# Optimization experiments

Measured on AMD Instinct MI355X. Metric: run time of the kernel, lower is better.

## Reference

```python
import jax, jax.numpy as jnp
import numpy as np

WINDOW = 128
BACKWARD = 1
FORWARD = 0

def look_around(x, pad_value):
    # x: [b, windows, window_size, ...]; pad window axis and gather shifted windows
    w = x.shape[1]
    pads = [(0, 0), (BACKWARD, FORWARD)] + [(0, 0)] * (x.ndim - 2)
    p = jnp.pad(x, pads, constant_values=pad_value)
    return jnp.concatenate([p[:, i:i + w] for i in range(BACKWARD + FORWARD + 1)], axis=2)

def setup_inputs() -> dict:
    key = jax.random.key(0)
    ks = jax.random.split(key, 5)
    shp = (2, 16, 4096, 64)
    names = ['q', 'k', 'q_rot', 'k_rot', 'v']
    inp = {n: jax.random.normal(ks[i], shp, dtype=jnp.float32) for i, n in enumerate(names)}
    inp['states'] = 0
    inp['inferring_states'] = 0
    return inp

def reference(q, k, q_rot, k_rot, v, states, inferring_states):
    shape = q.shape
    merge = lambda t: t.reshape(-1, t.shape[-2], t.shape[-1])
    q, k, q_rot, k_rot, v = map(merge, (q, k, q_rot, k_rot, v))
    b, t, e = q.shape
    windows = t // WINDOW
    ticker = jnp.arange(t, dtype=q.dtype)[None, :]
    b_t = ticker.reshape(1, windows, WINDOW)
    bucket = lambda x: x.reshape(b, windows, WINDOW, e)
    bq, bk, bq_rot, bk_rot, bv = map(bucket, (q, k, q_rot, k_rot, v))
    bk = look_around(bk, 0.0)
    bk_rot = look_around(bk_rot, 0.0)
    bv = look_around(bv, 0.0)
    bq_t = b_t
    bq_k = look_around(b_t, -1.0)
    scale = e ** (-0.5)
    dots = jnp.einsum('bwie,bwje->bwij', bq, bk) * scale
    dots_rot = jnp.einsum('bwie,bwje->bwij', bq_rot, bk_rot) * scale
    mask_value = -jnp.finfo(dots.dtype).max
    causal_mask = bq_t[:, :, :, None] < bq_k[:, :, None, :]
    pad_mask = bq_k[:, :, None, :] == -1
    mask = causal_mask | pad_mask
    dots = jnp.where(mask, mask_value, dots)
    dots_rot = jnp.where(mask, mask_value, dots_rot)
    attn = jax.nn.softmax(dots + dots_rot, axis=-1)
    out = jnp.einsum('bwij,bwje->bwie', attn, bv)
    return out.reshape(shape)
```

## Files before the change

### kernel.cpp

```cpp
#include <hip/hip_runtime.h>
#include <stdint.h>

#define T 4096
#define E 64
#define NBH 32
#define NWIN 32
#define LDKS 128
#define LDVS 64
#define KK_ELEMS (64*LDKS)
#define VT_ELEMS (64*LDVS)
#define BUF_ELEMS (KK_ELEMS+VT_ELEMS)
#define SMEM_BYTES (2*BUF_ELEMS*2)

typedef __attribute__((ext_vector_type(8))) short short8;
typedef __attribute__((ext_vector_type(4))) short short4v;
typedef __attribute__((ext_vector_type(4))) float f32x4;

__device__ __forceinline__ short f2bf(float x) {
  unsigned u = __float_as_uint(x);
  u += 0x7fffu + ((u >> 16) & 1u);
  return (short)(u >> 16);
}

__device__ __forceinline__ unsigned cvtpk(float lo, float hi) {
  unsigned r;
  asm("v_cvt_pk_bf16_f32 %0, %1, %2" : "=v"(r) : "v"(lo), "v"(hi));
  return r;
}

__device__ __forceinline__ void block_sync_lds() {
  asm volatile("s_waitcnt lgkmcnt(0)" ::: "memory");
  __builtin_amdgcn_s_barrier();
  asm volatile("" ::: "memory");
}

struct SubStage { float4 sk[4]; float sv[8]; };

__device__ __forceinline__ void sub_issue(SubStage& st,
    const float* __restrict__ k, const float* __restrict__ kr,
    const float* __restrict__ v, size_t rowbase, int tid, int wid, int lane) {
#pragma unroll
  for (int m = 0; m < 2; ++m) {
    const float* src = m ? kr : k;
#pragma unroll
    for (int it = 0; it < 2; ++it) {
      int idx = it * 512 + tid;
      st.sk[m * 2 + it] = *(const float4*)(src + (rowbase + (idx >> 4)) * E + (idx & 15) * 4);
    }
  }
  const float* vp = v + (rowbase + wid * 8) * E + lane;
#pragma unroll
  for (int i = 0; i < 8; ++i) st.sv[i] = vp[(size_t)i * E];
}

__device__ __forceinline__ void sub_commit(const SubStage& st,
    short* __restrict__ KK, short* __restrict__ Vt, int tid, int wid, int lane) {
#pragma unroll
  for (int m = 0; m < 2; ++m)
#pragma unroll
    for (int it = 0; it < 2; ++it) {
      int idx = it * 512 + tid;
      int row = idx >> 4;
      int chunk = m * 8 + ((idx & 15) >> 1);
      float4 f = st.sk[m * 2 + it];
      short4v h = { f2bf(f.x), f2bf(f.y), f2bf(f.z), f2bf(f.w) };
      *(short4v*)(KK + row * LDKS + ((chunk ^ (row & 15)) << 3) + (idx & 1) * 4) = h;
    }
#pragma unroll
  for (int rq = 0; rq < 2; ++rq) {
    short4v h = { f2bf(st.sv[rq*4+0]), f2bf(st.sv[rq*4+1]),
                  f2bf(st.sv[rq*4+2]), f2bf(st.sv[rq*4+3]) };
    *(short4v*)(Vt + lane * LDVS + ((wid ^ (lane & 7)) << 3) + rq * 4) = h;
  }
}

__device__ __forceinline__ void q_issue(float4* sq,
    const float* __restrict__ q, const float* __restrict__ qr,
    size_t rbase, int w, int wid, int li, int lg) {
  const size_t qrow = rbase + (size_t)w * 128 + wid * 16 + li;
#pragma unroll
  for (int kt = 0; kt < 4; ++kt) {
    const float* sp = (kt < 2 ? q : qr) + qrow * E + (kt & 1) * 32 + lg * 8;
    sq[kt * 2 + 0] = *(const float4*)sp;
    sq[kt * 2 + 1] = *(const float4*)(sp + 4);
  }
}

__device__ __forceinline__ void q_commit(const float4* sq, short8* aF) {
#pragma unroll
  for (int kt = 0; kt < 4; ++kt) {
    float4 f0 = sq[kt * 2], f1 = sq[kt * 2 + 1];
    short8 a;
    a[0]=f2bf(f0.x*0.125f); a[1]=f2bf(f0.y*0.125f); a[2]=f2bf(f0.z*0.125f); a[3]=f2bf(f0.w*0.125f);
    a[4]=f2bf(f1.x*0.125f); a[5]=f2bf(f1.y*0.125f); a[6]=f2bf(f1.z*0.125f); a[7]=f2bf(f1.w*0.125f);
    aF[kt] = a;
  }
}

__global__ __launch_bounds__(512, 4)
void la_attn(const float* __restrict__ qg, const float* __restrict__ kg,
             const float* __restrict__ qrg, const float* __restrict__ krg,
             const float* __restrict__ vg, float* __restrict__ outg) {
  extern __shared__ short smem[];

  const int lid = blockIdx.y * NWIN + blockIdx.x;
  const int wl  = (lid & 7) * 128 + (lid >> 3);
  const int win = wl & (NWIN - 1), bh = wl >> 5;

  const int tid = threadIdx.x;
  const int wid = tid >> 6, lane = tid & 63;
  const int li = lane & 15, lg = lane >> 4;
  const size_t rbase = (size_t)bh * T;
  const int q_i = wid * 16 + li;

  short8 aF[4];
  SubStage st;

  const int s0 = (win == 0) ? 2 : 0;
#define KROW(s) (rbase + (size_t)(win * 128 + ((s) - 2) * 64))

  {
    SubStage stA;
    float4 sq[8];
    sub_issue(stA, kg, krg, vg, KROW(s0), tid, wid, lane);
    q_issue(sq, qg, qrg, rbase, win, wid, li, lg);
    sub_commit(stA, smem, smem + KK_ELEMS, tid, wid, lane);
    q_commit(sq, aF);
    if (s0 + 1 < 4) sub_issue(st, kg, krg, vg, KROW(s0 + 1), tid, wid, lane);
  }
  block_sync_lds();

  float m = -1e30f, l = 0.f;
  f32x4 O[4] = {{0,0,0,0},{0,0,0,0},{0,0,0,0},{0,0,0,0}};

  for (int s = s0; s < 4; ++s) {
    const int cur = (s - s0) & 1;
    short* KKc = smem + cur * BUF_ELEMS;
    short* Vtc = KKc + KK_ELEMS;

    if (s + 1 < 4) {
      sub_commit(st, smem + (cur ^ 1) * BUF_ELEMS,
                 smem + (cur ^ 1) * BUF_ELEMS + KK_ELEMS, tid, wid, lane);
      if (s + 2 < 4) sub_issue(st, kg, krg, vg, KROW(s + 2), tid, wid, lane);
      asm volatile("" ::: "memory");
    }

    f32x4 p[4];
#pragma unroll
    for (int ct = 0; ct < 4; ++ct) {
      f32x4 acc = {0.f, 0.f, 0.f, 0.f};
      const int row = ct * 16 + li;
#pragma unroll
      for (int kt = 0; kt < 4; ++kt) {
        const short* kb = KKc + row * LDKS + (((kt * 4 + lg) ^ li) << 3);
        acc = __builtin_amdgcn_mfma_f32_16x16x32_bf16(*(const short8*)kb, aF[kt], acc, 0, 0, 0);
      }
      p[ct] = acc;
    }

    if (s >= 2) {
      const int joff = (s - 2) * 64 + lg * 4;
#pragma unroll
      for (int ct = 0; ct < 4; ++ct)
#pragma unroll
        for (int r = 0; r < 4; ++r)
          if (joff + ct * 16 + r > q_i) p[ct][r] = -1e30f;
    }
    float mx = -1e30f;
#pragma unroll
    for (int ct = 0; ct < 4; ++ct)
#pragma unroll
      for (int r = 0; r < 4; ++r) mx = fmaxf(mx, p[ct][r]);
    mx = fmaxf(mx, __shfl_xor(mx, 16));
    mx = fmaxf(mx, __shfl_xor(mx, 32));
    const float mn = fmaxf(m, mx);
    const float f = __expf(m - mn);
    float sm = 0.f;
#pragma unroll
    for (int ct = 0; ct < 4; ++ct)
#pragma unroll
      for (int r = 0; r < 4; ++r) {
        float e = __expf(p[ct][r] - mn);
        p[ct][r] = e;
        sm += e;
      }
    sm += __shfl_xor(sm, 16);
    sm += __shfl_xor(sm, 32);
    l = l * f + sm;
    m = mn;
#pragma unroll
    for (int nt = 0; nt < 4; ++nt)
#pragma unroll
      for (int r = 0; r < 4; ++r) O[nt][r] *= f;

    unsigned W0[4], W1[4];
#pragma unroll
    for (int ct = 0; ct < 4; ++ct) {
      W0[ct] = cvtpk(p[ct][0], p[ct][1]);
      W1[ct] = cvtpk(p[ct][2], p[ct][3]);
    }

    const bool lowhalf = (lg < 2);
    const bool sendR = (lg == 0) | (lg == 3);
#pragma unroll
    for (int kt = 0; kt < 2; ++kt) {
      const int cA = kt * 2, cB = cA + 1;
      unsigned P0 = lowhalf ? W0[cB] : W0[cA];
      unsigned P1 = lowhalf ? W1[cB] : W1[cA];
      unsigned R0 = __shfl_xor(P0, 32);
      unsigned R1 = __shfl_xor(P1, 32);
      unsigned L0 = lowhalf ? W0[cA] : W0[cB];
      unsigned L1 = lowhalf ? W1[cA] : W1[cB];
      unsigned S0 = sendR ? R0 : L0;
      unsigned S1 = sendR ? R1 : L1;
      unsigned T0 = __shfl_xor(S0, 16);
      unsigned T1 = __shfl_xor(S1, 16);
      unsigned F0 = (lg == 0) ? L0 : ((lg == 2) ? R0 : T0);
      unsigned F1 = (lg == 0) ? L1 : ((lg == 2) ? R1 : T1);
      unsigned G0 = (lg == 1) ? R0 : ((lg == 3) ? L0 : T0);
      unsigned G1 = (lg == 1) ? R1 : ((lg == 3) ? L1 : T1);
      union { unsigned u[4]; short8 s; } bu;
      bu.u[0] = F0; bu.u[1] = F1; bu.u[2] = G0; bu.u[3] = G1;
      const short8 bP = bu.s;
#pragma unroll
      for (int nt = 0; nt < 4; ++nt) {
        const short* vb = Vtc + (nt * 16 + li) * LDVS + (((kt * 4 + lg) ^ (li & 7)) << 3);
        O[nt] = __builtin_amdgcn_mfma_f32_16x16x32_bf16(*(const short8*)vb, bP, O[nt], 0, 0, 0);
      }
    }

    block_sync_lds();
  }

  const float linv = 1.f / l;
  float* op = outg + (rbase + (size_t)win * 128 + wid * 16 + li) * E + lg * 4;
#pragma unroll
  for (int nt = 0; nt < 4; ++nt) {
    float4 o = { O[nt][0] * linv, O[nt][1] * linv, O[nt][2] * linv, O[nt][3] * linv };
    *(float4*)(op + nt * 16) = o;
  }
#undef KROW
}

extern "C" void kernel_launch(void* const* d_in, const int* in_sizes, int n_in,
                              void* d_out, int out_size, void* d_ws, size_t ws_size,
                              hipStream_t stream) {
  const float* q  = (const float*)d_in[0];
  const float* k  = (const float*)d_in[1];
  const float* qr = (const float*)d_in[2];
  const float* kr = (const float*)d_in[3];
  const float* v  = (const float*)d_in[4];
  float* out = (float*)d_out;
  la_attn<<<dim3(NWIN, NBH), 512, SMEM_BYTES, stream>>>(q, k, qr, kr, v, out);
}
```

Baseline: 201.3 us.

## Drop LDS staging; read K directly, pre-transpose V to bf16 in separate kernel

```diff
diff --git a/kernel.cpp b/kernel.cpp
--- a/kernel.cpp
+++ b/kernel.cpp
@@ -5,15 +5,8 @@
 #define E 64
 #define NBH 32
 #define NWIN 32
-#define LDKS 128
-#define LDVS 64
-#define KK_ELEMS (64*LDKS)
-#define VT_ELEMS (64*LDVS)
-#define BUF_ELEMS (KK_ELEMS+VT_ELEMS)
-#define SMEM_BYTES (2*BUF_ELEMS*2)
 
 typedef __attribute__((ext_vector_type(8))) short short8;
-typedef __attribute__((ext_vector_type(4))) short short4v;
 typedef __attribute__((ext_vector_type(4))) float f32x4;
 
 __device__ __forceinline__ short f2bf(float x) {
@@ -28,218 +21,207 @@
   return r;
 }
 
-__device__ __forceinline__ void block_sync_lds() {
-  asm volatile("s_waitcnt lgkmcnt(0)" ::: "memory");
-  __builtin_amdgcn_s_barrier();
-  asm volatile("" ::: "memory");
-}
-
-struct SubStage { float4 sk[4]; float sv[8]; };
-
-__device__ __forceinline__ void sub_issue(SubStage& st,
-    const float* __restrict__ k, const float* __restrict__ kr,
-    const float* __restrict__ v, size_t rowbase, int tid, int wid, int lane) {
-#pragma unroll
-  for (int m = 0; m < 2; ++m) {
-    const float* src = m ? kr : k;
-#pragma unroll
-    for (int it = 0; it < 2; ++it) {
-      int idx = it * 512 + tid;
-      st.sk[m * 2 + it] = *(const float4*)(src + (rowbase + (idx >> 4)) * E + (idx & 15) * 4);
-    }
-  }
-  const float* vp = v + (rowbase + wid * 8) * E + lane;
-#pragma unroll
-  for (int i = 0; i < 8; ++i) st.sv[i] = vp[(size_t)i * E];
-}
-
-__device__ __forceinline__ void sub_commit(const SubStage& st,
-    short* __restrict__ KK, short* __restrict__ Vt, int tid, int wid, int lane) {
-#pragma unroll
-  for (int m = 0; m < 2; ++m)
-#pragma unroll
-    for (int it = 0; it < 2; ++it) {
-      int idx = it * 512 + tid;
-      int row = idx >> 4;
-      int chunk = m * 8 + ((idx & 15) >> 1);
-      float4 f = st.sk[m * 2 + it];
-      short4v h = { f2bf(f.x), f2bf(f.y), f2bf(f.z), f2bf(f.w) };
-      *(short4v*)(KK + row * LDKS + ((chunk ^ (row & 15)) << 3) + (idx & 1) * 4) = h;
-    }
-#pragma unroll
-  for (int rq = 0; rq < 2; ++rq) {
-    short4v h = { f2bf(st.sv[rq*4+0]), f2bf(st.sv[rq*4+1]),
-                  f2bf(st.sv[rq*4+2]), f2bf(st.sv[rq*4+3]) };
-    *(short4v*)(Vt + lane * LDVS + ((wid ^ (lane & 7)) << 3) + rq * 4) = h;
-  }
-}
-
-__device__ __forceinline__ void q_issue(float4* sq,
-    const float* __restrict__ q, const float* __restrict__ qr,
-    size_t rbase, int w, int wid, int li, int lg) {
-  const size_t qrow = rbase + (size_t)w * 128 + wid * 16 + li;
-#pragma unroll
-  for (int kt = 0; kt < 4; ++kt) {
-    const float* sp = (kt < 2 ? q : qr) + qrow * E + (kt & 1) * 32 + lg * 8;
-    sq[kt * 2 + 0] = *(const float4*)sp;
-    sq[kt * 2 + 1] = *(const float4*)(sp + 4);
-  }
-}
-
-__device__ __forceinline__ void q_commit(const float4* sq, short8* aF) {
-#pragma unroll
-  for (int kt = 0; kt < 4; ++kt) {
-    float4 f0 = sq[kt * 2], f1 = sq[kt * 2 + 1];
-    short8 a;
-    a[0]=f2bf(f0.x*0.125f); a[1]=f2bf(f0.y*0.125f); a[2]=f2bf(f0.z*0.125f); a[3]=f2bf(f0.w*0.125f);
-    a[4]=f2bf(f1.x*0.125f); a[5]=f2bf(f1.y*0.125f); a[6]=f2bf(f1.z*0.125f); a[7]=f2bf(f1.w*0.125f);
-    aF[kt] = a;
-  }
-}
-
-__global__ __launch_bounds__(512, 4)
+__device__ __forceinline__ short8 pack8(float4 f0, float4 f1) {
+  union { unsigned u[4]; short8 s8; } r;
+  r.u[0] = cvtpk(f0.x, f0.y); r.u[1] = cvtpk(f0.z, f0.w);
+  r.u[2] = cvtpk(f1.x, f1.y); r.u[3] = cvtpk(f1.z, f1.w);
+  return r.s8;
+}
+
+__device__ __forceinline__ short8 pack8s(float4 f0, float4 f1, float s) {
+  union { unsigned u[4]; short8 s8; } r;
+  r.u[0] = cvtpk(f0.x*s, f0.y*s); r.u[1] = cvtpk(f0.z*s, f0.w*s);
+  r.u[2] = cvtpk(f1.x*s, f1.y*s); r.u[3] = cvtpk(f1.z*s, f1.w*s);
+  return r.s8;
+}
+
+__global__ __launch_bounds__(256)
+void v_transpose(const float* __restrict__ vg, short* __restrict__ vt) {
+  __shared__ float tile[64][65];
+  const int bh = blockIdx.y;
+  const int t0 = blockIdx.x * 64;
+  const int tid = threadIdx.x;
+  const int c = tid & 63, r4 = tid >> 6;
+  const float* src = vg + ((size_t)bh * T + t0) * E;
+#pragma unroll
+  for (int i = 0; i < 16; ++i) {
+    int r = i * 4 + r4;
+    tile[r][c] = src[(size_t)r * E + c];
+  }
+  __syncthreads();
+  short* dst = vt + (size_t)bh * E * T + t0;
+#pragma unroll
+  for (int i = 0; i < 16; ++i) {
+    int e = i * 4 + r4;
+    dst[(size_t)e * T + c] = f2bf(tile[c][e]);
+  }
+}
+
+template<int KT>
+__device__ __forceinline__ short8 pv_bfrag(const unsigned* W0, const unsigned* W1, int lg) {
+  const bool lowhalf = (lg < 2);
+  const bool sendR = (lg == 0) | (lg == 3);
+  const int cA = KT * 2, cB = cA + 1;
+  unsigned P0 = lowhalf ? W0[cB] : W0[cA];
+  unsigned P1 = lowhalf ? W1[cB] : W1[cA];
+  unsigned R0 = __shfl_xor(P0, 32);
+  unsigned R1 = __shfl_xor(P1, 32);
+  unsigned L0 = lowhalf ? W0[cA] : W0[cB];
+  unsigned L1 = lowhalf ? W1[cA] : W1[cB];
+  unsigned S0 = sendR ? R0 : L0;
+  unsigned S1 = sendR ? R1 : L1;
+  unsigned T0 = __shfl_xor(S0, 16);
+  unsigned T1 = __shfl_xor(S1, 16);
+  unsigned F0 = (lg == 0) ? L0 : ((lg == 2) ? R0 : T0);
+  unsigned F1 = (lg == 0) ? L1 : ((lg == 2) ? R1 : T1);
+  unsigned G0 = (lg == 1) ? R0 : ((lg == 3) ? L0 : T0);
+  unsigned G1 = (lg == 1) ? R1 : ((lg == 3) ? L1 : T1);
+  union { unsigned u[4]; short8 s; } bu;
+  bu.u[0] = F0; bu.u[1] = F1; bu.u[2] = G0; bu.u[3] = G1;
+  return bu.s;
+}
+
+__global__ __launch_bounds__(256)
 void la_attn(const float* __restrict__ qg, const float* __restrict__ kg,
              const float* __restrict__ qrg, const float* __restrict__ krg,
-             const float* __restrict__ vg, float* __restrict__ outg) {
-  extern __shared__ short smem[];
-
+             const short* __restrict__ vtg, float* __restrict__ outg) {
   const int lid = blockIdx.y * NWIN + blockIdx.x;
   const int wl  = (lid & 7) * 128 + (lid >> 3);
   const int win = wl & (NWIN - 1), bh = wl >> 5;
 
   const int tid = threadIdx.x;
-  const int wid = tid >> 6, lane = tid & 63;
+  const int wv = tid >> 6, lane = tid & 63;
   const int li = lane & 15, lg = lane >> 4;
   const size_t rbase = (size_t)bh * T;
-  const int q_i = wid * 16 + li;
-
-  short8 aF[4];
-  SubStage st;
+  const int qb = wv * 32;
+
+  short8 aF[2][4];
+#pragma unroll
+  for (int qt = 0; qt < 2; ++qt) {
+    const size_t qrow = rbase + (size_t)win * 128 + qb + qt * 16 + li;
+#pragma unroll
+    for (int kt = 0; kt < 4; ++kt) {
+      const float* sp = (kt < 2 ? qg : qrg) + qrow * E + (kt & 1) * 32 + lg * 8;
+      float4 f0 = *(const float4*)sp, f1 = *(const float4*)(sp + 4);
+      aF[qt][kt] = pack8s(f0, f1, 0.125f);
+    }
+  }
+
+  float m[2] = {-1e30f, -1e30f}, l[2] = {0.f, 0.f};
+  f32x4 O[2][4];
+#pragma unroll
+  for (int qt = 0; qt < 2; ++qt)
+#pragma unroll
+    for (int nt = 0; nt < 4; ++nt) O[qt][nt] = f32x4{0.f, 0.f, 0.f, 0.f};
 
   const int s0 = (win == 0) ? 2 : 0;
-#define KROW(s) (rbase + (size_t)(win * 128 + ((s) - 2) * 64))
-
-  {
-    SubStage stA;
-    float4 sq[8];
-    sub_issue(stA, kg, krg, vg, KROW(s0), tid, wid, lane);
-    q_issue(sq, qg, qrg, rbase, win, wid, li, lg);
-    sub_commit(stA, smem, smem + KK_ELEMS, tid, wid, lane);
-    q_commit(sq, aF);
-    if (s0 + 1 < 4) sub_issue(st, kg, krg, vg, KROW(s0 + 1), tid, wid, lane);
-  }
-  block_sync_lds();
-
-  float m = -1e30f, l = 0.f;
-  f32x4 O[4] = {{0,0,0,0},{0,0,0,0},{0,0,0,0},{0,0,0,0}};
 
   for (int s = s0; s < 4; ++s) {
-    const int cur = (s - s0) & 1;
-    short* KKc = smem + cur * BUF_ELEMS;
-    short* Vtc = KKc + KK_ELEMS;
-
-    if (s + 1 < 4) {
-      sub_commit(st, smem + (cur ^ 1) * BUF_ELEMS,
-                 smem + (cur ^ 1) * BUF_ELEMS + KK_ELEMS, tid, wid, lane);
-      if (s + 2 < 4) sub_issue(st, kg, krg, vg, KROW(s + 2), tid, wid, lane);
-      asm volatile("" ::: "memory");
-    }
-
-    f32x4 p[4];
+    const int tloc = win * 128 + (s - 2) * 64;
+    const size_t keyb = rbase + tloc;
+
+    f32x4 p[2][4];
+#pragma unroll
+    for (int qt = 0; qt < 2; ++qt)
+#pragma unroll
+      for (int ct = 0; ct < 4; ++ct) p[qt][ct] = f32x4{0.f, 0.f, 0.f, 0.f};
 #pragma unroll
     for (int ct = 0; ct < 4; ++ct) {
-      f32x4 acc = {0.f, 0.f, 0.f, 0.f};
-      const int row = ct * 16 + li;
-#pragma unroll
-      for (int kt = 0; kt < 4; ++kt) {
-        const short* kb = KKc + row * LDKS + (((kt * 4 + lg) ^ li) << 3);
-        acc = __builtin_amdgcn_mfma_f32_16x16x32_bf16(*(const short8*)kb, aF[kt], acc, 0, 0, 0);
-      }
-      p[ct] = acc;
-    }
-
-    if (s >= 2) {
-      const int joff = (s - 2) * 64 + lg * 4;
+      const float* rk = kg  + (keyb + ct * 16 + li) * E + lg * 8;
+      const float* rr = krg + (keyb + ct * 16 + li) * E + lg * 8;
+      float4 a0 = *(const float4*)(rk);      float4 a1 = *(const float4*)(rk + 4);
+      float4 b0 = *(const float4*)(rk + 32); float4 b1 = *(const float4*)(rk + 36);
+      float4 c0 = *(const float4*)(rr);      float4 c1 = *(const float4*)(rr + 4);
+      float4 d0 = *(const float4*)(rr + 32); float4 d1 = *(const float4*)(rr + 36);
+      short8 kA0 = pack8(a0, a1), kA1 = pack8(b0, b1);
+      short8 kA2 = pack8(c0, c1), kA3 = pack8(d0, d1);
+#pragma unroll
+      for (int qt = 0; qt < 2; ++qt) {
+        p[qt][ct] = __builtin_amdgcn_mfma_f32_16x16x32_bf16(kA0, aF[qt][0], p[qt][ct], 0, 0, 0);
+        p[qt][ct] = __builtin_amdgcn_mfma_f32_16x16x32_bf16(kA1, aF[qt][1], p[qt][ct], 0, 0, 0);
+        p[qt][ct] = __builtin_amdgcn_mfma_f32_16x16x32_bf16(kA2, aF[qt][2], p[qt][ct], 0, 0, 0);
+        p[qt][ct] = __builtin_amdgcn_mfma_f32_16x16x32_bf16(kA3, aF[qt][3], p[qt][ct], 0, 0, 0);
+      }
+    }
+
+    short8 vA[2][4];
+#pragma unroll
+    for (int kt = 0; kt < 2; ++kt)
+#pragma unroll
+      for (int nt = 0; nt < 4; ++nt)
+        vA[kt][nt] = *(const short8*)(vtg + ((size_t)bh * E + nt * 16 + li) * T
+                                          + tloc + kt * 32 + lg * 8);
+
+#pragma unroll
+    for (int qt = 0; qt < 2; ++qt) {
+      const int q_i = qb + qt * 16 + li;
+      if (s >= 2) {
+        const int joff = (s - 2) * 64 + lg * 4;
+#pragma unroll
+        for (int ct = 0; ct < 4; ++ct)
+#pragma unroll
+          for (int r = 0; r < 4; ++r)
+            if (joff + ct * 16 + r > q_i) p[qt][ct][r] = -1e30f;
+      }
+      float mx = -1e30f;
 #pragma unroll
       for (int ct = 0; ct < 4; ++ct)
 #pragma unroll
-        for (int r = 0; r < 4; ++r)
-          if (joff + ct * 16 + r > q_i) p[ct][r] = -1e30f;
-    }
-    float mx = -1e30f;
-#pragma unroll
-    for (int ct = 0; ct < 4; ++ct)
-#pragma unroll
-      for (int r = 0; r < 4; ++r) mx = fmaxf(mx, p[ct][r]);
-    mx = fmaxf(mx, __shfl_xor(mx, 16));
-    mx = fmaxf(mx, __shfl_xor(mx, 32));
-    const float mn = fmaxf(m, mx);
-    const float f = __expf(m - mn);
-    float sm = 0.f;
-#pragma unroll
-    for (int ct = 0; ct < 4; ++ct)
-#pragma unroll
-      for (int r = 0; r < 4; ++r) {
-        float e = __expf(p[ct][r] - mn);
-        p[ct][r] = e;
-        sm += e;
-      }
-    sm += __shfl_xor(sm, 16);
-    sm += __shfl_xor(sm, 32);
-    l = l * f + sm;
-    m = mn;
-#pragma unroll
-    for (int nt = 0; nt < 4; ++nt)
-#pragma unroll
-      for (int r = 0; r < 4; ++r) O[nt][r] *= f;
-
-    unsigned W0[4], W1[4];
-#pragma unroll
-    for (int ct = 0; ct < 4; ++ct) {
-      W0[ct] = cvtpk(p[ct][0], p[ct][1]);
-      W1[ct] = cvtpk(p[ct][2], p[ct][3]);
-    }
-
-    const bool lowhalf = (lg < 2);
-    const bool sendR = (lg == 0) | (lg == 3);
-#pragma unroll
-    for (int kt = 0; kt < 2; ++kt) {
-      const int cA = kt * 2, cB = cA + 1;
-      unsigned P0 = lowhalf ? W0[cB] : W0[cA];
-      unsigned P1 = lowhalf ? W1[cB] : W1[cA];
-      unsigned R0 = __shfl_xor(P0, 32);
-      unsigned R1 = __shfl_xor(P1, 32);
-      unsigned L0 = lowhalf ? W0[cA] : W0[cB];
-      unsigned L1 = lowhalf ? W1[cA] : W1[cB];
-      unsigned S0 = sendR ? R0 : L0;
-      unsigned S1 = sendR ? R1 : L1;
-      unsigned T0 = __shfl_xor(S0, 16);
-      unsigned T1 = __shfl_xor(S1, 16);
-      unsigned F0 = (lg == 0) ? L0 : ((lg == 2) ? R0 : T0);
-      unsigned F1 = (lg == 0) ? L1 : ((lg == 2) ? R1 : T1);
-      unsigned G0 = (lg == 1) ? R0 : ((lg == 3) ? L0 : T0);
-      unsigned G1 = (lg == 1) ? R1 : ((lg == 3) ? L1 : T1);
-      union { unsigned u[4]; short8 s; } bu;
-      bu.u[0] = F0; bu.u[1] = F1; bu.u[2] = G0; bu.u[3] = G1;
-      const short8 bP = bu.s;
-#pragma unroll
-      for (int nt = 0; nt < 4; ++nt) {
-        const short* vb = Vtc + (nt * 16 + li) * LDVS + (((kt * 4 + lg) ^ (li & 7)) << 3);
-        O[nt] = __builtin_amdgcn_mfma_f32_16x16x32_bf16(*(const short8*)vb, bP, O[nt], 0, 0, 0);
-      }
-    }
-
-    block_sync_lds();
-  }
-
-  const float linv = 1.f / l;
-  float* op = outg + (rbase + (size_t)win * 128 + wid * 16 + li) * E + lg * 4;
-#pragma unroll
-  for (int nt = 0; nt < 4; ++nt) {
-    float4 o = { O[nt][0] * linv, O[nt][1] * linv, O[nt][2] * linv, O[nt][3] * linv };
-    *(float4*)(op + nt * 16) = o;
-  }
-#undef KROW
+        for (int r = 0; r < 4; ++r) mx = fmaxf(mx, p[qt][ct][r]);
+      mx = fmaxf(mx, __shfl_xor(mx, 16));
+      mx = fmaxf(mx, __shfl_xor(mx, 32));
+      const float mn = fmaxf(m[qt], mx);
+      const float f = __expf(m[qt] - mn);
+      float sm = 0.f;
+#pragma unroll
+      for (int ct = 0; ct < 4; ++ct)
+#pragma unroll
+        for (int r = 0; r < 4; ++r) {
+          float e = __expf(p[qt][ct][r] - mn);
+          p[qt][ct][r] = e;
+          sm += e;
+        }
+      sm += __shfl_xor(sm, 16);
+      sm += __shfl_xor(sm, 32);
+      l[qt] = l[qt] * f + sm;
+      m[qt] = mn;
+#pragma unroll
+      for (int nt = 0; nt < 4; ++nt)
+#pragma unroll
+        for (int r = 0; r < 4; ++r) O[qt][nt][r] *= f;
+
+      unsigned W0[4], W1[4];
+#pragma unroll
+      for (int ct = 0; ct < 4; ++ct) {
+        W0[ct] = cvtpk(p[qt][ct][0], p[qt][ct][1]);
+        W1[ct] = cvtpk(p[qt][ct][2], p[qt][ct][3]);
+      }
+      {
+        const short8 bP0 = pv_bfrag<0>(W0, W1, lg);
+#pragma unroll
+        for (int nt = 0; nt < 4; ++nt)
+          O[qt][nt] = __builtin_amdgcn_mfma_f32_16x16x32_bf16(vA[0][nt], bP0, O[qt][nt], 0, 0, 0);
+      }
+      {
+        const short8 bP1 = pv_bfrag<1>(W0, W1, lg);
+#pragma unroll
+        for (int nt = 0; nt < 4; ++nt)
+          O[qt][nt] = __builtin_amdgcn_mfma_f32_16x16x32_bf16(vA[1][nt], bP1, O[qt][nt], 0, 0, 0);
+      }
+    }
+  }
+
+#pragma unroll
+  for (int qt = 0; qt < 2; ++qt) {
+    const float linv = 1.f / l[qt];
+    float* op = outg + (rbase + (size_t)win * 128 + qb + qt * 16 + li) * E + lg * 4;
+#pragma unroll
+    for (int nt = 0; nt < 4; ++nt) {
+      float4 o = { O[qt][nt][0] * linv, O[qt][nt][1] * linv,
+                   O[qt][nt][2] * linv, O[qt][nt][3] * linv };
+      *(float4*)(op + nt * 16) = o;
+    }
+  }
 }
 
 extern "C" void kernel_launch(void* const* d_in, const int* in_sizes, int n_in,
@@ -251,5 +233,7 @@
   const float* kr = (const float*)d_in[3];
   const float* v  = (const float*)d_in[4];
   float* out = (float*)d_out;
-  la_attn<<<dim3(NWIN, NBH), 512, SMEM_BYTES, stream>>>(q, k, qr, kr, v, out);
-}
+  short* vt = (short*)d_ws;
+  v_transpose<<<dim3(T / 64, NBH), 256, 0, stream>>>(v, vt);
+  la_attn<<<dim3(NWIN, NBH), 256, 0, stream>>>(q, k, qr, kr, vt, out);
+}
```

New measurement: 256.5 us. 27.4% more time.
